# Kernel optimization log

Measured on AMD Instinct MI355X. Metric: run time of the kernel, lower is better.

## Reference

```python
import jax, jax.numpy as jnp
import numpy as np

N = 100000      # num nodes
F_IN = 512      # dataset.num_features
HID = 32        # hardcoded hidden dim in CRD
C = 40          # dataset.num_classes
E = 3200000     # num edges


def setup_inputs() -> dict:
    key = jax.random.key(0)
    ks = jax.random.split(key, 16)
    def glorot(k, shape):
        lim = float(np.sqrt(6.0 / (shape[0] + shape[1])))
        return jax.random.uniform(k, shape, jnp.float32, -lim, lim)
    inp = {
        "x": jax.random.normal(ks[0], (N, F_IN), dtype=jnp.float32),
        "edge_index": jax.random.randint(ks[1], (2, E), 0, N, dtype=jnp.int32),
        # CRD 1: two GCNConv(F_IN -> HID)
        "W1a": glorot(ks[2], (F_IN, HID)), "b1a": jnp.zeros((HID,), jnp.float32),
        "W1b": glorot(ks[3], (F_IN, HID)), "b1b": jnp.zeros((HID,), jnp.float32),
        # CRD 2: two GCNConv(F_IN -> HID)
        "W2a": glorot(ks[4], (F_IN, HID)), "b2a": jnp.zeros((HID,), jnp.float32),
        "W2b": glorot(ks[5], (F_IN, HID)), "b2b": jnp.zeros((HID,), jnp.float32),
        # CLS: two GCNConv(HID -> C)
        "W3a": glorot(ks[6], (HID, C)), "b3a": jnp.zeros((C,), jnp.float32),
        "W3b": glorot(ks[7], (HID, C)), "b3b": jnp.zeros((C,), jnp.float32),
    }
    return inp


def reference(x, edge_index, W1a, b1a, W1b, b1b, W2a, b2a, W2b, b2b, W3a, b3a, W3b, b3b):
    n = x.shape[0]
    # GCN normalization with self-loops (PyG gcn_norm, cached=True -> shared)
    loop = jnp.arange(n, dtype=edge_index.dtype)
    src = jnp.concatenate([edge_index[0], loop])  # [E+N]
    dst = jnp.concatenate([edge_index[1], loop])
    deg = jax.ops.segment_sum(jnp.ones_like(dst, jnp.float32), dst, num_segments=n)
    dinv = jnp.where(deg > 0, jax.lax.rsqrt(jnp.maximum(deg, 1e-12)), 0.0)
    norm = dinv[src] * dinv[dst]  # [E+N]

    def gcn(h, W, b):
        hw = h @ W                                     # [n, d_out] project first
        msg = hw[src] * norm[:, None]                  # gather + scale
        return jax.ops.segment_sum(msg, dst, num_segments=n) + b  # scatter-add

    # CRD 1 (dropout is identity in eval)
    x1 = jax.nn.relu(gcn(x, W1a, b1a)) + jax.nn.relu(gcn(x, W1b, b1b))
    # CRD 2
    x2 = jax.nn.relu(gcn(x, W2a, b2a)) + jax.nn.relu(gcn(x, W2b, b2b))
    # CLS
    xs = x1 + x2
    out = jax.nn.log_softmax(gcn(xs, W3a, b3a) + gcn(xs, W3b, b3b), axis=1)
    return out
```

## Files before the change

### kernel.cpp

```cpp
#include <hip/hip_runtime.h>
#include <hip/hip_bf16.h>
#include <math.h>

typedef __attribute__((ext_vector_type(8))) short short8;
typedef __attribute__((ext_vector_type(4))) float f32x4;

__device__ inline ushort f2bf(float f) {
    uint u = __builtin_bit_cast(uint, f);
    u += 0x7fffu + ((u >> 16) & 1u);
    return (ushort)(u >> 16);
}
__device__ inline float bf2f(ushort h) {
    return __builtin_bit_cast(float, (uint)h << 16);
}


#define NB   256
#define BKE  2048
#define CAP  16384
#define MAXBE 16384

__device__ inline int bucket_of(int d, int W, float recipW) {
    int g = (int)((float)d * recipW);
    if (g > NB - 1) g = NB - 1;
    while (d < g * W) --g;
    while (d >= (g + 1) * W) ++g;
    return g;
}

__global__ __launch_bounds__(256) void bucket_kernel(const int* __restrict__ src, const int* __restrict__ dst,
                                                     int* __restrict__ cursor256, int* __restrict__ epk,
                                                     int E, int W, float recipW) {
    __shared__ int hist[NB];
    __shared__ int base[NB];
    int tid = threadIdx.x;
    int e0 = blockIdx.x * BKE;
    int e1 = e0 + BKE; if (e1 > E) e1 = E;
    if (e0 >= E) return;
    hist[tid] = 0;
    __syncthreads();
    int myp[8], myg[8], myr[8];
    #pragma unroll
    for (int it = 0; it < 8; ++it) {
        int e = e0 + tid + it * 256;
        myg[it] = -1;
        if (e < e1) {
            int d = dst[e];
            int g = bucket_of(d, W, recipW);
            myp[it] = src[e] | ((d - g * W) << 17);
            myg[it] = g;
            myr[it] = atomicAdd(&hist[g], 1);
        }
    }
    __syncthreads();
    base[tid] = atomicAdd(&cursor256[tid], hist[tid]);
    __syncthreads();
    #pragma unroll
    for (int it = 0; it < 8; ++it)
        if (myg[it] >= 0)
            epk[base[myg[it]] + myr[it]] = myp[it];
}

__global__ void scanpost_kernel(const int* __restrict__ cursor256, int* __restrict__ bbase) {
    __shared__ int tot[NB];
    int b = threadIdx.x;
    int cnt = cursor256[b] - b * CAP;
    tot[b] = cnt;
    __syncthreads();
    for (int off = 1; off < NB; off <<= 1) {
        int t = (b >= off) ? tot[b - off] : 0;
        __syncthreads();
        tot[b] += t;
        __syncthreads();
    }
    bbase[b] = tot[b] - cnt;
    if (b == NB - 1) bbase[NB] = tot[NB - 1];
}

__global__ __launch_bounds__(256) void sortcsr_kernel(const int* __restrict__ epk,
                                                      const int* __restrict__ bbase,
                                                      int* __restrict__ csr, int* __restrict__ offs,
                                                      float* __restrict__ dinv, int N, int W, int E) {
    __shared__ int lcnt[512];
    __shared__ int lofs[513];
    __shared__ int tmp[256];
    __shared__ int lcsr[MAXBE];
    int b = blockIdx.x;
    int lo = b * W;
    int nloc = N - lo; if (nloc > W) nloc = W; if (nloc < 0) nloc = 0;
    int gbase = bbase[b];
    int cnt = bbase[b + 1] - gbase;
    int ebk = b * CAP;
    int tid = threadIdx.x;
    lcnt[2 * tid] = 0; lcnt[2 * tid + 1] = 0;
    __syncthreads();
    for (int e = tid; e < cnt; e += 256)
        atomicAdd(&lcnt[epk[ebk + e] >> 17], 1);
    __syncthreads();
    int a0 = lcnt[2 * tid], a1 = lcnt[2 * tid + 1];
    int psum = a0 + a1;
    tmp[tid] = psum;
    __syncthreads();
    for (int off = 1; off < 256; off <<= 1) {
        int t = (tid >= off) ? tmp[tid - off] : 0;
        __syncthreads();
        tmp[tid] += t;
        __syncthreads();
    }
    int excl = tmp[tid] - psum;
    lofs[2 * tid] = excl;
    lofs[2 * tid + 1] = excl + a0;
    lcnt[2 * tid] = excl;
    lcnt[2 * tid + 1] = excl + a0;
    if (tid == 255) lofs[512] = tmp[255];
    __syncthreads();
    for (int t = tid; t < nloc; t += 256) {
        offs[lo + t] = gbase + lofs[t];
        int deg = lofs[t + 1] - lofs[t];
        dinv[lo + t] = rsqrtf((float)(deg + 1));
    }
    if (b == NB - 1 && tid == 0) offs[N] = E;
    for (int e = tid; e < cnt; e += 256) {
        int p = epk[ebk + e];
        int pos = atomicAdd(&lcnt[p >> 17], 1);
        int sv = p & 0x1FFFF;
        if (pos < MAXBE) lcsr[pos] = sv;
        else csr[gbase + pos] = sv;
    }
    __syncthreads();
    int ne = cnt; if (ne > MAXBE) ne = MAXBE;
    for (int e = tid; e < ne; e += 256) csr[gbase + e] = lcsr[e];
}


__global__ __launch_bounds__(256) void prep_kernel(const float* __restrict__ W1a, const float* __restrict__ W1b,
                                                   const float* __restrict__ W2a, const float* __restrict__ W2b,
                                                   const float* __restrict__ b1a, const float* __restrict__ b1b,
                                                   const float* __restrict__ b2a, const float* __restrict__ b2b,
                                                   const float* __restrict__ W3a, const float* __restrict__ W3b,
                                                   const float* __restrict__ b3a, const float* __restrict__ b3b,
                                                   ushort* __restrict__ Wt, float* __restrict__ bcat,
                                                   float* __restrict__ W3s, float* __restrict__ b3s,
                                                   int* __restrict__ cursor256) {
    int idx = blockIdx.x * 256 + threadIdx.x;
    if (blockIdx.x == 0) cursor256[threadIdx.x] = threadIdx.x * CAP;
    if (idx < 128 * 512) {
        int row = idx >> 9, kk = idx & 511;
        int cstore = (kk >> 3) & 7;
        int clog = cstore ^ (row & 7);
        int klog = (kk & ~63) | (clog << 3) | (kk & 7);
        const float* Wsrc = (row < 32) ? W1a : (row < 64) ? W1b : (row < 96) ? W2a : W2b;
        Wt[idx] = f2bf(Wsrc[klog * 32 + (row & 31)]);
    }
    if (idx < 1280) W3s[idx] = W3a[idx] + W3b[idx];
    if (idx < 128) {
        const float* b = (idx < 32) ? b1a : (idx < 64) ? b1b : (idx < 96) ? b2a : b2b;
        bcat[idx] = b[idx & 31];
    }
    if (idx < 40) b3s[idx] = b3a[idx] + b3b[idx];
}


#define GBM 64

__global__ __launch_bounds__(256) void gemm_mfma(const float* __restrict__ X,
                                                 const ushort* __restrict__ Wt,
                                                 const float* __restrict__ dinv,
                                                 ushort* __restrict__ HWp, int N) {
    __shared__ float  Af[64 * 64];
    __shared__ ushort Bl[128 * 64];
    const int tid = threadIdx.x;
    const int lane = tid & 63;
    const int wave = tid >> 6;
    const int rQ = lane & 15, g = lane >> 4;
    const int rowBase = blockIdx.x * GBM;

    const float* agsrc[4];
    #pragma unroll
    for (int i = 0; i < 4; ++i) {
        int q = (i * 4 + wave) * 64 + lane;
        int row = q >> 4, c = q & 15;
        int rowg = rowBase + row; if (rowg > N - 1) rowg = N - 1;
        agsrc[i] = X + (size_t)rowg * 512 + ((c ^ (row & 15)) << 2);
    }
    const ushort* bgsrc[4];
    #pragma unroll
    for (int i = 0; i < 4; ++i) {
        int q = (i * 4 + wave) * 64 + lane;
        int row = q >> 3, c = q & 7;
        bgsrc[i] = Wt + (size_t)row * 512 + (c << 3);
    }

    f32x4 acc[4][2] = {};

#define STAGE(s)                                                              \
    {                                                                         \
        _Pragma("unroll")                                                     \
        for (int i = 0; i < 4; ++i)                                           \
            __builtin_amdgcn_global_load_lds(                                 \
                (const uint*)(agsrc[i] + (s) * 64),                           \
                (uint*)&Af[(i * 4 + wave) * 256], 16, 0, 0);                  \
        _Pragma("unroll")                                                     \
        for (int i = 0; i < 4; ++i)                                           \
            __builtin_amdgcn_global_load_lds(                                 \
                (const uint*)(bgsrc[i] + (s) * 64),                           \
                (uint*)&Bl[(i * 4 + wave) * 512], 16, 0, 0);                  \
    }

#define COMPUTE()                                                             \
    {                                                                         \
        short8 bfr[2][2];                                                     \
        _Pragma("unroll")                                                     \
        for (int ct2 = 0; ct2 < 2; ++ct2) {                                   \
            int brow = wave * 32 + ct2 * 16 + rQ;                             \
            _Pragma("unroll")                                                 \
            for (int sub = 0; sub < 2; ++sub)                                 \
                bfr[ct2][sub] = *(const short8*)(&Bl[brow * 64 + (((sub * 4 + g) ^ (brow & 7)) << 3)]); \
        }                                                                     \
        _Pragma("unroll")                                                     \
        for (int rt = 0; rt < 4; ++rt) {                                      \
            int arw = rt * 16 + rQ;                                           \
            _Pragma("unroll")                                                 \
            for (int sub = 0; sub < 2; ++sub) {                               \
                int c0 = (sub * 4 + g) * 2;                                   \
                float4 lo = *(const float4*)(&Af[arw * 64 + ((c0 ^ (arw & 15)) << 2)]);       \
                float4 hi = *(const float4*)(&Af[arw * 64 + (((c0 + 1) ^ (arw & 15)) << 2)]); \
                union { short8 s8; __hip_bfloat162 h[4]; } u;                 \
                u.h[0] = __float22bfloat162_rn({lo.x, lo.y});                 \
                u.h[1] = __float22bfloat162_rn({lo.z, lo.w});                 \
                u.h[2] = __float22bfloat162_rn({hi.x, hi.y});                 \
                u.h[3] = __float22bfloat162_rn({hi.z, hi.w});                 \
                _Pragma("unroll")                                             \
                for (int ct2 = 0; ct2 < 2; ++ct2)                             \
                    acc[rt][ct2] = __builtin_amdgcn_mfma_f32_16x16x32_bf16(   \
                        u.s8, bfr[ct2][sub], acc[rt][ct2], 0, 0, 0);          \
            }                                                                 \
        }                                                                     \
    }

    for (int s = 0; s < 8; ++s) {
        STAGE(s);
        __syncthreads();
        COMPUTE();
        __syncthreads();
    }

    #pragma unroll
    for (int rt = 0; rt < 4; ++rt) {
        #pragma unroll
        for (int j = 0; j < 4; ++j) {
            int r = rowBase + rt * 16 + g * 4 + j;
            if (r < N) {
                float dv = dinv[r];
                #pragma unroll
                for (int ct2 = 0; ct2 < 2; ++ct2) {
                    int c = wave * 32 + ct2 * 16 + rQ;
                    HWp[(size_t)r * 128 + c] = f2bf(acc[rt][ct2][j] * dv);
                }
            }
        }
    }
#undef STAGE
#undef COMPUTE
}


__global__ __launch_bounds__(256) void agg128(const ushort* __restrict__ HWp, const float* __restrict__ dinv,
                                              const int* __restrict__ offs, const int* __restrict__ csr,
                                              const float* __restrict__ bcat, ushort* __restrict__ xsp, int N) {
    int t = blockIdx.x * 256 + threadIdx.x;
    int node = t >> 4, c = t & 15;
    if (node >= N) return;
    const short8* H = (const short8*)HWp;
    short8 h = H[(size_t)node * 16 + c];
    float a[8];
    #pragma unroll
    for (int i = 0; i < 8; ++i) a[i] = bf2f((ushort)h[i]);
    int j = offs[node];
    int e1 = offs[node + 1];
    int jend = j + ((e1 - j) & ~7);
    for (; j < jend; j += 8) {
        int s[8];
        #pragma unroll
        for (int q = 0; q < 8; ++q) s[q] = csr[j + q];
        short8 v[8];
        #pragma unroll
        for (int q = 0; q < 8; ++q) v[q] = H[(size_t)s[q] * 16 + c];
        #pragma unroll
        for (int q = 0; q < 8; ++q)
            #pragma unroll
            for (int i = 0; i < 8; ++i) a[i] += bf2f((ushort)v[q][i]);
    }
    for (; j < e1; ++j) {
        short8 v = H[(size_t)csr[j] * 16 + c];
        #pragma unroll
        for (int i = 0; i < 8; ++i) a[i] += bf2f((ushort)v[i]);
    }
    float di = dinv[node];
    float4 b0 = *(const float4*)(bcat + c * 8);
    float4 b1 = *(const float4*)(bcat + c * 8 + 4);
    float bb[8] = {b0.x, b0.y, b0.z, b0.w, b1.x, b1.y, b1.z, b1.w};
    float r[8];
    #pragma unroll
    for (int i = 0; i < 8; ++i) r[i] = fmaxf(di * a[i] + bb[i], 0.f);
    #pragma unroll
    for (int i = 0; i < 8; ++i) { r[i] += __shfl_xor(r[i], 4); r[i] += __shfl_xor(r[i], 8); }
    if ((c & 12) == 0) {
        union { short8 s8; ushort us[8]; } o;
        #pragma unroll
        for (int i = 0; i < 8; ++i) o.us[i] = f2bf(r[i] * di);
        *(short8*)(xsp + (size_t)node * 32 + c * 8) = o.s8;
    }
}


__global__ __launch_bounds__(256) void agg32f(const ushort* __restrict__ xsp, const float* __restrict__ dinv,
                                              const int* __restrict__ offs, const int* __restrict__ csr,
                                              const float* __restrict__ W3s, const float* __restrict__ b3s,
                                              float* __restrict__ out, int N) {
    __shared__ float w[32 * 40];
    __shared__ float bsh[40];
    int tid = threadIdx.x;
    for (int i = tid; i < 1280; i += 256) w[i] = W3s[i];
    if (tid < 40) bsh[tid] = b3s[tid];
    __syncthreads();

    int t = blockIdx.x * 256 + tid;
    int node = t >> 2, l = t & 3;
    if (node >= N) return;
    const short8* Xr = (const short8*)xsp;
    short8 h = Xr[(size_t)node * 4 + l];
    float a[8];
    #pragma unroll
    for (int i = 0; i < 8; ++i) a[i] = bf2f((ushort)h[i]);
    int j = offs[node];
    int e1 = offs[node + 1];
    int jend = j + ((e1 - j) & ~7);
    for (; j < jend; j += 8) {
        int s[8];
        #pragma unroll
        for (int q = 0; q < 8; ++q) s[q] = csr[j + q];
        short8 v[8];
        #pragma unroll
        for (int q = 0; q < 8; ++q) v[q] = Xr[(size_t)s[q] * 4 + l];
        #pragma unroll
        for (int q = 0; q < 8; ++q)
            #pragma unroll
            for (int i = 0; i < 8; ++i) a[i] += bf2f((ushort)v[q][i]);
    }
    for (; j < e1; ++j) {
        short8 v = Xr[(size_t)csr[j] * 4 + l];
        #pragma unroll
        for (int i = 0; i < 8; ++i) a[i] += bf2f((ushort)v[i]);
    }
    float di = dinv[node];

    float lg[40];
    #pragma unroll
    for (int c = 0; c < 40; ++c) lg[c] = 0.f;
    #pragma unroll
    for (int k = 0; k < 8; ++k) {
        float av = a[k] * di;
        const float* wr = &w[(l * 8 + k) * 40];
        #pragma unroll
        for (int c = 0; c < 40; ++c) lg[c] += av * wr[c];
    }
    #pragma unroll
    for (int c = 0; c < 40; ++c) {
        lg[c] += __shfl_xor(lg[c], 1);
        lg[c] += __shfl_xor(lg[c], 2);
        lg[c] += bsh[c];
    }
    float m = lg[0];
    #pragma unroll
    for (int c = 1; c < 40; ++c) m = fmaxf(m, lg[c]);
    float sum = 0.f;
    #pragma unroll
    for (int c = 0; c < 40; ++c) sum += expf(lg[c] - m);
    float lgs = m + logf(sum);
    bool lo1 = (l & 1), hi2 = (l & 2);
    float* op = out + (size_t)node * 40 + l * 10;
    #pragma unroll
    for (int c = 0; c < 10; ++c) {
        float va = lo1 ? lg[10 + c] : lg[c];
        float vb = lo1 ? lg[30 + c] : lg[20 + c];
        float v  = hi2 ? vb : va;
        op[c] = v - lgs;
    }
}


extern "C" void kernel_launch(void* const* d_in, const int* in_sizes, int n_in,
                              void* d_out, int out_size, void* d_ws, size_t ws_size,
                              hipStream_t stream) {
    const float* x   = (const float*)d_in[0];
    const int*   ei  = (const int*)d_in[1];
    const float* W1a = (const float*)d_in[2];  const float* b1a = (const float*)d_in[3];
    const float* W1b = (const float*)d_in[4];  const float* b1b = (const float*)d_in[5];
    const float* W2a = (const float*)d_in[6];  const float* b2a = (const float*)d_in[7];
    const float* W2b = (const float*)d_in[8];  const float* b2b = (const float*)d_in[9];
    const float* W3a = (const float*)d_in[10]; const float* b3a = (const float*)d_in[11];
    const float* W3b = (const float*)d_in[12]; const float* b3b = (const float*)d_in[13];

    int N = in_sizes[0] / 512;
    int E = in_sizes[1] / 2;
    const int* srcv = ei;
    const int* dstv = ei + E;
    int W = (N + NB - 1) / NB;
    float recipW = 1.0f / (float)W;

    char* ws = (char*)d_ws;
    size_t off = 0;
    auto alloc = [&](size_t bytes) { void* p = ws + off; off = (off + bytes + 255) & ~(size_t)255; return p; };
    int*    offs     = (int*)   alloc((size_t)(N + 1) * 4);
    float*  dinv     = (float*) alloc((size_t)N * 4);
    int*    bbase    = (int*)   alloc((NB + 1) * 4);
    int*    cursor256= (int*)   alloc(NB * 4);
    int*    csr      = (int*)   alloc((size_t)E * 4);
    ushort* Wt       = (ushort*)alloc(128 * 512 * 2);
    float*  bcat     = (float*) alloc(128 * 4);
    float*  W3s      = (float*) alloc(1280 * 4);
    float*  b3s      = (float*) alloc(40 * 4);
    ushort* HWp      = (ushort*)alloc((size_t)N * 128 * 2);
    ushort* xsp      = (ushort*)alloc((size_t)N * 32 * 2);

    int* epk = (int*)HWp;

    prep_kernel<<<256, 256, 0, stream>>>(W1a, W1b, W2a, W2b, b1a, b1b, b2a, b2b,
                                         W3a, W3b, b3a, b3b, Wt, bcat, W3s, b3s, cursor256);
    bucket_kernel<<<(E + BKE - 1) / BKE, 256, 0, stream>>>(srcv, dstv, cursor256, epk, E, W, recipW);
    scanpost_kernel<<<1, 256, 0, stream>>>(cursor256, bbase);
    sortcsr_kernel<<<NB, 256, 0, stream>>>(epk, bbase, csr, offs, dinv, N, W, E);
    gemm_mfma<<<(N + GBM - 1) / GBM, 256, 0, stream>>>(x, Wt, dinv, HWp, N);
    agg128<<<((size_t)N * 16 + 255) / 256, 256, 0, stream>>>(HWp, dinv, offs, csr, bcat, xsp, N);
    agg32f<<<((size_t)N * 4 + 255) / 256, 256, 0, stream>>>(xsp, dinv, offs, csr, W3s, b3s,
                                                            (float*)d_out, N);
}
```

Measured before the change: 302.1 us.

## Shrink GEMM K-tile, vectorize bucket loads, fold scan into sortcsr

Three changes: bucket_kernel reads src/dst with 16-byte vector loads plus a scalar tail, the separate scanpost kernel is removed and each sortcsr block recomputes the 256-entry prefix scan itself, and the MFMA GEMM halves its K tile (32 instead of 64) with matching swizzles and double the stage count. The aims are fewer launches, better load efficiency, and lower LDS use per block for higher occupancy. The cost is more barrier-separated K iterations in the GEMM and a redundant scan in every sortcsr block.

New measurement: 311.6 us. 3.1% more time.

```diff
diff --git a/kernel.cpp b/kernel.cpp
--- a/kernel.cpp
+++ b/kernel.cpp
@@ -4,6 +4,7 @@
 
 typedef __attribute__((ext_vector_type(8))) short short8;
 typedef __attribute__((ext_vector_type(4))) float f32x4;
+typedef __attribute__((ext_vector_type(4))) int i32x4;
 
 __device__ inline ushort f2bf(float f) {
     uint u = __builtin_bit_cast(uint, f);
@@ -23,6 +24,7 @@
 __device__ inline int bucket_of(int d, int W, float recipW) {
     int g = (int)((float)d * recipW);
     if (g > NB - 1) g = NB - 1;
+    if (g < 0) g = 0;
     while (d < g * W) --g;
     while (d >= (g + 1) * W) ++g;
     return g;
@@ -35,50 +37,53 @@
     __shared__ int base[NB];
     int tid = threadIdx.x;
     int e0 = blockIdx.x * BKE;
+    if (e0 >= E) return;
     int e1 = e0 + BKE; if (e1 > E) e1 = E;
-    if (e0 >= E) return;
+    int n4 = (e1 - e0) >> 2;
     hist[tid] = 0;
     __syncthreads();
+    const i32x4* d4 = (const i32x4*)(dst + e0);
+    const i32x4* s4 = (const i32x4*)(src + e0);
     int myp[8], myg[8], myr[8];
     #pragma unroll
-    for (int it = 0; it < 8; ++it) {
-        int e = e0 + tid + it * 256;
-        myg[it] = -1;
-        if (e < e1) {
-            int d = dst[e];
-            int g = bucket_of(d, W, recipW);
-            myp[it] = src[e] | ((d - g * W) << 17);
-            myg[it] = g;
-            myr[it] = atomicAdd(&hist[g], 1);
+    for (int i = 0; i < 2; ++i) {
+        int q = i * 256 + tid;
+        if (q < n4) {
+            i32x4 dv = d4[q];
+            i32x4 sv = s4[q];
+            #pragma unroll
+            for (int j = 0; j < 4; ++j) {
+                int d = dv[j];
+                int g = bucket_of(d, W, recipW);
+                myp[i * 4 + j] = sv[j] | ((d - g * W) << 17);
+                myg[i * 4 + j] = g;
+                myr[i * 4 + j] = atomicAdd(&hist[g], 1);
+            }
+        } else {
+            #pragma unroll
+            for (int j = 0; j < 4; ++j) myg[i * 4 + j] = -1;
         }
     }
+    int tg = -1, tp = 0, tr = 0;
+    for (int e = e0 + n4 * 4 + tid; e < e1; e += 256) {
+        int d = dst[e];
+        int g = bucket_of(d, W, recipW);
+        tp = src[e] | ((d - g * W) << 17);
+        tg = g;
+        tr = atomicAdd(&hist[g], 1);
+    }
     __syncthreads();
     base[tid] = atomicAdd(&cursor256[tid], hist[tid]);
     __syncthreads();
     #pragma unroll
-    for (int it = 0; it < 8; ++it)
-        if (myg[it] >= 0)
-            epk[base[myg[it]] + myr[it]] = myp[it];
-}
-
-__global__ void scanpost_kernel(const int* __restrict__ cursor256, int* __restrict__ bbase) {
-    __shared__ int tot[NB];
-    int b = threadIdx.x;
-    int cnt = cursor256[b] - b * CAP;
-    tot[b] = cnt;
-    __syncthreads();
-    for (int off = 1; off < NB; off <<= 1) {
-        int t = (b >= off) ? tot[b - off] : 0;
-        __syncthreads();
-        tot[b] += t;
-        __syncthreads();
-    }
-    bbase[b] = tot[b] - cnt;
-    if (b == NB - 1) bbase[NB] = tot[NB - 1];
+    for (int i = 0; i < 8; ++i)
+        if (myg[i] >= 0)
+            epk[base[myg[i]] + myr[i]] = myp[i];
+    if (tg >= 0) epk[base[tg] + tr] = tp;
 }
 
 __global__ __launch_bounds__(256) void sortcsr_kernel(const int* __restrict__ epk,
-                                                      const int* __restrict__ bbase,
+                                                      const int* __restrict__ cursor256,
                                                       int* __restrict__ csr, int* __restrict__ offs,
                                                       float* __restrict__ dinv, int N, int W, int E) {
     __shared__ int lcnt[512];
@@ -88,11 +93,20 @@
     int b = blockIdx.x;
     int lo = b * W;
     int nloc = N - lo; if (nloc > W) nloc = W; if (nloc < 0) nloc = 0;
-    int gbase = bbase[b];
-    int cnt = bbase[b + 1] - gbase;
     int ebk = b * CAP;
     int tid = threadIdx.x;
     lcnt[2 * tid] = 0; lcnt[2 * tid + 1] = 0;
+    tmp[tid] = cursor256[tid] - tid * CAP;
+    __syncthreads();
+    for (int off = 1; off < 256; off <<= 1) {
+        int t = (tid >= off) ? tmp[tid - off] : 0;
+        __syncthreads();
+        tmp[tid] += t;
+        __syncthreads();
+    }
+    int incl = tmp[b];
+    int cnt = (b == 0) ? incl : incl - tmp[b - 1];
+    int gbase = incl - cnt;
     __syncthreads();
     for (int e = tid; e < cnt; e += 256)
         atomicAdd(&lcnt[epk[ebk + e] >> 17], 1);
@@ -146,9 +160,9 @@
     if (blockIdx.x == 0) cursor256[threadIdx.x] = threadIdx.x * CAP;
     if (idx < 128 * 512) {
         int row = idx >> 9, kk = idx & 511;
-        int cstore = (kk >> 3) & 7;
-        int clog = cstore ^ (row & 7);
-        int klog = (kk & ~63) | (clog << 3) | (kk & 7);
+        int cstore = (kk >> 3) & 3;
+        int clog = cstore ^ (row & 3);
+        int klog = (kk & ~31) | (clog << 3) | (kk & 7);
         const float* Wsrc = (row < 32) ? W1a : (row < 64) ? W1b : (row < 96) ? W2a : W2b;
         Wt[idx] = f2bf(Wsrc[klog * 32 + (row & 31)]);
     }
@@ -167,27 +181,27 @@
                                                  const ushort* __restrict__ Wt,
                                                  const float* __restrict__ dinv,
                                                  ushort* __restrict__ HWp, int N) {
-    __shared__ float  Af[64 * 64];
-    __shared__ ushort Bl[128 * 64];
+    __shared__ float  Af[64 * 32];
+    __shared__ ushort Bl[128 * 32];
     const int tid = threadIdx.x;
     const int lane = tid & 63;
     const int wave = tid >> 6;
     const int rQ = lane & 15, g = lane >> 4;
     const int rowBase = blockIdx.x * GBM;
 
-    const float* agsrc[4];
-    #pragma unroll
-    for (int i = 0; i < 4; ++i) {
-        int q = (i * 4 + wave) * 64 + lane;
-        int row = q >> 4, c = q & 15;
-        int rowg = rowBase + row; if (rowg > N - 1) rowg = N - 1;
-        agsrc[i] = X + (size_t)rowg * 512 + ((c ^ (row & 15)) << 2);
-    }
-    const ushort* bgsrc[4];
-    #pragma unroll
-    for (int i = 0; i < 4; ++i) {
+    const float* agsrc[2];
+    #pragma unroll
+    for (int i = 0; i < 2; ++i) {
         int q = (i * 4 + wave) * 64 + lane;
         int row = q >> 3, c = q & 7;
+        int rowg = rowBase + row; if (rowg > N - 1) rowg = N - 1;
+        agsrc[i] = X + (size_t)rowg * 512 + ((c ^ (row & 7)) << 2);
+    }
+    const ushort* bgsrc[2];
+    #pragma unroll
+    for (int i = 0; i < 2; ++i) {
+        int q = (i * 4 + wave) * 64 + lane;
+        int row = q >> 2, c = q & 3;
         bgsrc[i] = Wt + (size_t)row * 512 + (c << 3);
     }
 
@@ -196,49 +210,43 @@
 #define STAGE(s)                                                              \
     {                                                                         \
         _Pragma("unroll")                                                     \
-        for (int i = 0; i < 4; ++i)                                           \
+        for (int i = 0; i < 2; ++i)                                           \
             __builtin_amdgcn_global_load_lds(                                 \
-                (const uint*)(agsrc[i] + (s) * 64),                           \
+                (const uint*)(agsrc[i] + (s) * 32),                           \
                 (uint*)&Af[(i * 4 + wave) * 256], 16, 0, 0);                  \
         _Pragma("unroll")                                                     \
-        for (int i = 0; i < 4; ++i)                                           \
+        for (int i = 0; i < 2; ++i)                                           \
             __builtin_amdgcn_global_load_lds(                                 \
-                (const uint*)(bgsrc[i] + (s) * 64),                           \
+                (const uint*)(bgsrc[i] + (s) * 32),                           \
                 (uint*)&Bl[(i * 4 + wave) * 512], 16, 0, 0);                  \
     }
 
 #define COMPUTE()                                                             \
     {                                                                         \
-        short8 bfr[2][2];                                                     \
+        short8 bfr[2];                                                        \
         _Pragma("unroll")                                                     \
         for (int ct2 = 0; ct2 < 2; ++ct2) {                                   \
             int brow = wave * 32 + ct2 * 16 + rQ;                             \
-            _Pragma("unroll")                                                 \
-            for (int sub = 0; sub < 2; ++sub)                                 \
-                bfr[ct2][sub] = *(const short8*)(&Bl[brow * 64 + (((sub * 4 + g) ^ (brow & 7)) << 3)]); \
+            bfr[ct2] = *(const short8*)(&Bl[brow * 32 + ((g ^ (brow & 3)) << 3)]); \
         }                                                                     \
         _Pragma("unroll")                                                     \
         for (int rt = 0; rt < 4; ++rt) {                                      \
             int arw = rt * 16 + rQ;                                           \
+            float4 lo = *(const float4*)(&Af[arw * 32 + (((2 * g) ^ (arw & 7)) << 2)]);     \
+            float4 hi = *(const float4*)(&Af[arw * 32 + (((2 * g + 1) ^ (arw & 7)) << 2)]); \
+            union { short8 s8; __hip_bfloat162 h[4]; } u;                     \
+            u.h[0] = __float22bfloat162_rn({lo.x, lo.y});                     \
+            u.h[1] = __float22bfloat162_rn({lo.z, lo.w});                     \
+            u.h[2] = __float22bfloat162_rn({hi.x, hi.y});                     \
+            u.h[3] = __float22bfloat162_rn({hi.z, hi.w});                     \
             _Pragma("unroll")                                                 \
-            for (int sub = 0; sub < 2; ++sub) {                               \
-                int c0 = (sub * 4 + g) * 2;                                   \
-                float4 lo = *(const float4*)(&Af[arw * 64 + ((c0 ^ (arw & 15)) << 2)]);       \
-                float4 hi = *(const float4*)(&Af[arw * 64 + (((c0 + 1) ^ (arw & 15)) << 2)]); \
-                union { short8 s8; __hip_bfloat162 h[4]; } u;                 \
-                u.h[0] = __float22bfloat162_rn({lo.x, lo.y});                 \
-                u.h[1] = __float22bfloat162_rn({lo.z, lo.w});                 \
-                u.h[2] = __float22bfloat162_rn({hi.x, hi.y});                 \
-                u.h[3] = __float22bfloat162_rn({hi.z, hi.w});                 \
-                _Pragma("unroll")                                             \
-                for (int ct2 = 0; ct2 < 2; ++ct2)                             \
-                    acc[rt][ct2] = __builtin_amdgcn_mfma_f32_16x16x32_bf16(   \
-                        u.s8, bfr[ct2][sub], acc[rt][ct2], 0, 0, 0);          \
-            }                                                                 \
+            for (int ct2 = 0; ct2 < 2; ++ct2)                                 \
+                acc[rt][ct2] = __builtin_amdgcn_mfma_f32_16x16x32_bf16(       \
+                    u.s8, bfr[ct2], acc[rt][ct2], 0, 0, 0);                   \
         }                                                                     \
     }
 
-    for (int s = 0; s < 8; ++s) {
+    for (int s = 0; s < 16; ++s) {
         STAGE(s);
         __syncthreads();
         COMPUTE();
@@ -414,7 +422,6 @@
     auto alloc = [&](size_t bytes) { void* p = ws + off; off = (off + bytes + 255) & ~(size_t)255; return p; };
     int*    offs     = (int*)   alloc((size_t)(N + 1) * 4);
     float*  dinv     = (float*) alloc((size_t)N * 4);
-    int*    bbase    = (int*)   alloc((NB + 1) * 4);
     int*    cursor256= (int*)   alloc(NB * 4);
     int*    csr      = (int*)   alloc((size_t)E * 4);
     ushort* Wt       = (ushort*)alloc(128 * 512 * 2);
@@ -429,8 +436,7 @@
     prep_kernel<<<256, 256, 0, stream>>>(W1a, W1b, W2a, W2b, b1a, b1b, b2a, b2b,
                                          W3a, W3b, b3a, b3b, Wt, bcat, W3s, b3s, cursor256);
     bucket_kernel<<<(E + BKE - 1) / BKE, 256, 0, stream>>>(srcv, dstv, cursor256, epk, E, W, recipW);
-    scanpost_kernel<<<1, 256, 0, stream>>>(cursor256, bbase);
-    sortcsr_kernel<<<NB, 256, 0, stream>>>(epk, bbase, csr, offs, dinv, N, W, E);
+    sortcsr_kernel<<<NB, 256, 0, stream>>>(epk, cursor256, csr, offs, dinv, N, W, E);
     gemm_mfma<<<(N + GBM - 1) / GBM, 256, 0, stream>>>(x, Wt, dinv, HWp, N);
     agg128<<<((size_t)N * 16 + 255) / 256, 256, 0, stream>>>(HWp, dinv, offs, csr, bcat, xsp, N);
     agg32f<<<((size_t)N * 4 + 255) / 256, 256, 0, stream>>>(xsp, dinv, offs, csr, W3s, b3s,
```
